# Kernel optimization log

Hardware: AMD Instinct MI355X
Metric: run time of the kernel (lower is better)

## Reference

```python
import jax, jax.numpy as jnp
import numpy as np

B, N, D = 1, 65536, 1024
H = 512
R = 16  # num_regions
C = 2   # num_classes

def _gelu(x):
    return jax.nn.gelu(x, approximate=False)  # torch nn.GELU default is exact erf

def setup_inputs() -> dict:
    key = jax.random.key(0)
    ks = jax.random.split(key, 16)
    s = 0.02
    return {
        "embeddings": jax.random.normal(ks[0], (B, N, D), dtype=jnp.float32),
        # region_encoder: Linear(D,H) + GELU (dropout=0 in eval)
        "W1": jax.random.normal(ks[1], (D, H), dtype=jnp.float32) * s,
        "b1": jnp.zeros((H,), dtype=jnp.float32),
        # region_attention: Linear(H,H//2) -> tanh -> Linear(H//2,1)
        "Wa1": jax.random.normal(ks[2], (H, H // 2), dtype=jnp.float32) * s,
        "ba1": jnp.zeros((H // 2,), dtype=jnp.float32),
        "Wa2": jax.random.normal(ks[3], (H // 2, 1), dtype=jnp.float32) * s,
        "ba2": jnp.zeros((1,), dtype=jnp.float32),
        # slide_encoder: Linear(H,H) + GELU
        "Ws": jax.random.normal(ks[4], (H, H), dtype=jnp.float32) * s,
        "bs": jnp.zeros((H,), dtype=jnp.float32),
        # slide_attention
        "Wsa1": jax.random.normal(ks[5], (H, H // 2), dtype=jnp.float32) * s,
        "bsa1": jnp.zeros((H // 2,), dtype=jnp.float32),
        "Wsa2": jax.random.normal(ks[6], (H // 2, 1), dtype=jnp.float32) * s,
        "bsa2": jnp.zeros((1,), dtype=jnp.float32),
        # classifier: Linear(H,H//2) -> GELU -> Linear(H//2,C)
        "Wc1": jax.random.normal(ks[7], (H, H // 2), dtype=jnp.float32) * s,
        "bc1": jnp.zeros((H // 2,), dtype=jnp.float32),
        "Wc2": jax.random.normal(ks[8], (H // 2, C), dtype=jnp.float32) * s,
        "bc2": jnp.zeros((C,), dtype=jnp.float32),
    }

def reference(embeddings, W1, b1, Wa1, ba1, Wa2, ba2, Ws, bs, Wsa1, bsa1, Wsa2, bsa2, Wc1, bc1, Wc2, bc2):
    b, n, d = embeddings.shape
    m = n // R  # patches per region
    # coords=None path: region_ids[i] = i % R, so region r holds indices r, r+R, ...
    # Equivalent regrouping via reshape+transpose: (B, M, R, D) -> (B, R, M, D)
    x = embeddings.reshape(b, m, R, d).transpose(0, 2, 1, 3)
    # region encoder
    region_emb = _gelu(jnp.einsum('brmd,dh->brmh', x, W1) + b1)  # (B,R,M,H)
    # region attention pooling
    scores = jnp.einsum('brmk,ko->brmo', jnp.tanh(jnp.einsum('brmh,hk->brmk', region_emb, Wa1) + ba1), Wa2) + ba2  # (B,R,M,1)
    attn = jax.nn.softmax(scores, axis=2)
    region_features = jnp.sum(region_emb * attn, axis=2)  # (B,R,H)
    # slide encoder + attention pooling over regions
    slide_emb = _gelu(jnp.einsum('brh,hg->brg', region_features, Ws) + bs)  # (B,R,H)
    sattn = jnp.einsum('brk,ko->bro', jnp.tanh(jnp.einsum('brh,hk->brk', slide_emb, Wsa1) + bsa1), Wsa2) + bsa2  # (B,R,1)
    sweights = jax.nn.softmax(sattn, axis=1)
    slide_rep = jnp.sum(slide_emb * sweights, axis=1)  # (B,H)
    # classifier
    logits = _gelu(slide_rep @ Wc1 + bc1) @ Wc2 + bc2  # (B,C)
    return logits
```

## Files before the change

kernel.cpp:

```cpp
#include <hip/hip_runtime.h>

#define NTOK 65536
#define DIN  1024
#define H    512
#define HH   256
#define NREG 16
#define MPR  4096

__device__ __forceinline__ unsigned short f2bf(float f) {
  unsigned u = __float_as_uint(f);
  u += 0x7fffu + ((u >> 16) & 1u);
  return (unsigned short)(u >> 16);
}
__device__ __forceinline__ float bf2f(unsigned short s) {
  return __uint_as_float(((unsigned)s) << 16);
}
__device__ __forceinline__ float gelu_exact(float x) {
  return 0.5f * x * (1.0f + erff(x * 0.70710678118654752440f));
}
__device__ __forceinline__ unsigned cvt_pk_bf16(float lo, float hi) {
  unsigned r;
  asm("v_cvt_pk_bf16_f32 %0, %1, %2" : "=v"(r) : "v"(lo), "v"(hi));
  return r;
}
__device__ __forceinline__ unsigned short f2bf_hw(float f) {
  unsigned r;
  asm("v_cvt_pk_bf16_f32 %0, %1, %2" : "=v"(r) : "v"(f), "v"(f));
  return (unsigned short)r;
}
__device__ __forceinline__ float fast_tanh(float x) {
  float e = __expf(2.0f * x);
  return 1.0f - 2.0f * __builtin_amdgcn_rcpf(e + 1.0f);
}

typedef __attribute__((ext_vector_type(8))) short shortx8;
typedef __attribute__((ext_vector_type(4))) float floatx4;
typedef __attribute__((ext_vector_type(4))) unsigned int uintx4;

__device__ __forceinline__ void gl_lds16(const void* g, void* l) {
  __builtin_amdgcn_global_load_lds(
      (const __attribute__((address_space(1))) void*)g,
      (__attribute__((address_space(3))) void*)l, 16, 0, 0);
}

__device__ __forceinline__ int swz8(int row, int seg) {
  return (row * 4 + (seg ^ ((row >> 1) & 3))) * 8;
}

__global__ __launch_bounds__(256) void k0_prep(const float* __restrict__ W1,
                                               const float* __restrict__ Wa1,
                                               unsigned short* __restrict__ W1t,
                                               unsigned short* __restrict__ Wa1t) {
  int idx = blockIdx.x * 256 + threadIdx.x;
  if (idx < DIN * H) {
    int n = idx >> 10, k = idx & 1023;
    W1t[idx] = f2bf(W1[k * H + n]);
  } else {
    int i2 = idx - DIN * H;
    int n = i2 >> 9, k = i2 & 511;
    Wa1t[i2] = f2bf(Wa1[k * HH + n]);
  }
}

__global__ __launch_bounds__(512) void k1_gemm1(const float* __restrict__ X,
                                                const unsigned short* __restrict__ W1t,
                                                const float* __restrict__ b1,
                                                unsigned short* __restrict__ Eb) {
  __shared__ __align__(16) short lA[128 * 32];
  __shared__ __align__(16) short lB[512 * 32];
  const int tid = threadIdx.x;
  const int rowBase = blockIdx.x * 128;
  const int lane = tid & 63;
  const int wave = tid >> 6;
  const int wr = wave >> 2, wc = wave & 3;
  const int l15 = lane & 15, quad = lane >> 4;

  floatx4 acc[4][8] = {};

  const int arow = tid >> 2, aseg = tid & 3;
  const float* aSrc = X + (size_t)(rowBase + arow) * DIN + aseg * 8;
  short* aDst = &lA[swz8(arow, aseg)];

  for (int kb = 0; kb < DIN; kb += 32) {
    __syncthreads();
#pragma unroll
    for (int s = 0; s < 4; s++) {
      int c = tid + s * 512;
      int n = c >> 2, slot = c & 3;
      int seg = slot ^ ((n >> 1) & 3);
      gl_lds16(W1t + (size_t)n * DIN + kb + seg * 8, &lB[c * 8]);
    }
    {
      const floatx4* src = (const floatx4*)(aSrc + kb);
      floatx4 f0 = src[0], f1 = src[1];
      uintx4 u;
      u[0] = cvt_pk_bf16(f0[0], f0[1]);
      u[1] = cvt_pk_bf16(f0[2], f0[3]);
      u[2] = cvt_pk_bf16(f1[0], f1[1]);
      u[3] = cvt_pk_bf16(f1[2], f1[3]);
      *(uintx4*)aDst = u;
    }
    __syncthreads();
    shortx8 aF[4], bF[8];
#pragma unroll
    for (int i = 0; i < 4; i++) {
      int r = wr * 64 + i * 16 + l15;
      aF[i] = *(const shortx8*)(&lA[swz8(r, quad)]);
    }
#pragma unroll
    for (int j = 0; j < 8; j++) {
      int r = wc * 128 + j * 16 + l15;
      bF[j] = *(const shortx8*)(&lB[swz8(r, quad)]);
    }
#pragma unroll
    for (int i = 0; i < 4; i++)
#pragma unroll
      for (int j = 0; j < 8; j++)
        acc[i][j] = __builtin_amdgcn_mfma_f32_16x16x32_bf16(aF[i], bF[j], acc[i][j], 0, 0, 0);
  }

  const int row0 = rowBase + wr * 64;
#pragma unroll
  for (int j = 0; j < 8; j++) {
    int col = wc * 128 + j * 16 + l15;
    float bias = b1[col];
#pragma unroll
    for (int i = 0; i < 4; i++) {
      int rb = row0 + i * 16 + quad * 4;
#pragma unroll
      for (int v = 0; v < 4; v++) {
        float x = acc[i][j][v] + bias;
        Eb[(size_t)(rb + v) * H + col] = f2bf_hw(gelu_exact(x));
      }
    }
  }
}

__global__ __launch_bounds__(256) void k2_gemm2(const unsigned short* __restrict__ Eb,
                                                const unsigned short* __restrict__ Wa1t,
                                                const float* __restrict__ ba1,
                                                const float* __restrict__ Wa2,
                                                float* __restrict__ scores) {
  __shared__ __align__(16) short lA[128 * 32];
  __shared__ __align__(16) short lB[128 * 32];
  const int tid = threadIdx.x;
  const int colBase = blockIdx.x * 128;
  const int rowBase = blockIdx.y * 128;
  const int lane = tid & 63;
  const int wave = tid >> 6;
  const int wr = wave >> 1, wc = wave & 1;
  const int l15 = lane & 15, quad = lane >> 4;

  floatx4 acc[4][4] = {};

  for (int kb = 0; kb < H; kb += 32) {
    __syncthreads();
#pragma unroll
    for (int s = 0; s < 2; s++) {
      int c = tid + s * 256;
      int n = c >> 2, slot = c & 3;
      int seg = slot ^ ((n >> 1) & 3);
      gl_lds16(Eb + (size_t)(rowBase + n) * H + kb + seg * 8, &lA[c * 8]);
      gl_lds16(Wa1t + (size_t)(colBase + n) * H + kb + seg * 8, &lB[c * 8]);
    }
    __syncthreads();
    shortx8 aF[4], bF[4];
#pragma unroll
    for (int i = 0; i < 4; i++) {
      int r = wr * 64 + i * 16 + l15;
      aF[i] = *(const shortx8*)(&lA[swz8(r, quad)]);
    }
#pragma unroll
    for (int j = 0; j < 4; j++) {
      int r = wc * 64 + j * 16 + l15;
      bF[j] = *(const shortx8*)(&lB[swz8(r, quad)]);
    }
#pragma unroll
    for (int i = 0; i < 4; i++)
#pragma unroll
      for (int j = 0; j < 4; j++)
        acc[i][j] = __builtin_amdgcn_mfma_f32_16x16x32_bf16(aF[i], bF[j], acc[i][j], 0, 0, 0);
  }

  float p[4][4];
#pragma unroll
  for (int i = 0; i < 4; i++)
#pragma unroll
    for (int v = 0; v < 4; v++) p[i][v] = 0.0f;
#pragma unroll
  for (int j = 0; j < 4; j++) {
    int col = colBase + wc * 64 + j * 16 + l15;
    float bias = ba1[col];
    float wa2 = Wa2[col];
#pragma unroll
    for (int i = 0; i < 4; i++)
#pragma unroll
      for (int v = 0; v < 4; v++)
        p[i][v] += fast_tanh(acc[i][j][v] + bias) * wa2;
  }
#pragma unroll
  for (int i = 0; i < 4; i++)
#pragma unroll
    for (int v = 0; v < 4; v++) {
      float t = p[i][v];
      t += __shfl_xor(t, 1, 16);
      t += __shfl_xor(t, 2, 16);
      t += __shfl_xor(t, 4, 16);
      t += __shfl_xor(t, 8, 16);
      p[i][v] = t;
    }
  if (l15 == 0) {
    int row0 = rowBase + wr * 64 + quad * 4;
#pragma unroll
    for (int i = 0; i < 4; i++)
#pragma unroll
      for (int v = 0; v < 4; v++)
        atomicAdd(&scores[row0 + i * 16 + v], p[i][v]);
  }
}

__global__ __launch_bounds__(256) void k3a_softmax(const float* __restrict__ scores,
                                                   float* __restrict__ wts) {
  const int r = blockIdx.x, tid = threadIdx.x;
  __shared__ float red[256];
  float m = -1e30f;
  for (int j = tid; j < MPR; j += 256) m = fmaxf(m, scores[r + NREG * j]);
  red[tid] = m;
  __syncthreads();
  for (int s = 128; s > 0; s >>= 1) {
    if (tid < s) red[tid] = fmaxf(red[tid], red[tid + s]);
    __syncthreads();
  }
  float mx = red[0];
  __syncthreads();
  float sum = 0.0f;
  for (int j = tid; j < MPR; j += 256) sum += expf(scores[r + NREG * j] - mx);
  red[tid] = sum;
  __syncthreads();
  for (int s = 128; s > 0; s >>= 1) {
    if (tid < s) red[tid] += red[tid + s];
    __syncthreads();
  }
  float inv = 1.0f / red[0];
  for (int j = tid; j < MPR; j += 256)
    wts[r + NREG * j] = expf(scores[r + NREG * j] - mx) * inv;
}

__global__ __launch_bounds__(256) void k3b_wsum(const unsigned short* __restrict__ Eb,
                                                const float* __restrict__ wts,
                                                float* __restrict__ rf) {
  const int r = blockIdx.y;
  const int mc = blockIdx.x;
  const int tid = threadIdx.x;
  float a0 = 0.0f, a1 = 0.0f;
  for (int j = mc * 128; j < mc * 128 + 128; j++) {
    int n = r + NREG * j;
    float w = wts[n];
    unsigned v = *(const unsigned*)(Eb + (size_t)n * H + tid * 2);
    a0 += w * bf2f((unsigned short)(v & 0xffffu));
    a1 += w * bf2f((unsigned short)(v >> 16));
  }
  atomicAdd(&rf[r * H + tid * 2], a0);
  atomicAdd(&rf[r * H + tid * 2 + 1], a1);
}

__global__ __launch_bounds__(256) void k4a_slide(const float* __restrict__ rf,
                                                 const float* __restrict__ Ws,
                                                 const float* __restrict__ bs,
                                                 float* __restrict__ se) {
  const int r = blockIdx.x, tid = threadIdx.x;
  __shared__ float lrf[H];
  lrf[tid] = rf[r * H + tid];
  lrf[tid + 256] = rf[r * H + tid + 256];
  __syncthreads();
  float a0 = 0.0f, a1 = 0.0f;
  for (int k = 0; k < H; k++) {
    float x = lrf[k];
    a0 += x * Ws[k * H + tid];
    a1 += x * Ws[k * H + tid + 256];
  }
  se[r * H + tid] = gelu_exact(a0 + bs[tid]);
  se[r * H + tid + 256] = gelu_exact(a1 + bs[tid + 256]);
}

__global__ __launch_bounds__(256) void k4b_sscore(const float* __restrict__ se,
                                                  const float* __restrict__ Wsa1,
                                                  const float* __restrict__ bsa1,
                                                  const float* __restrict__ Wsa2,
                                                  const float* __restrict__ bsa2,
                                                  float* __restrict__ ss) {
  const int r = blockIdx.x, tid = threadIdx.x;
  __shared__ float lse[H];
  __shared__ float red[256];
  lse[tid] = se[r * H + tid];
  lse[tid + 256] = se[r * H + tid + 256];
  __syncthreads();
  float a = 0.0f;
  for (int k = 0; k < H; k++) a += lse[k] * Wsa1[k * HH + tid];
  red[tid] = tanhf(a + bsa1[tid]) * Wsa2[tid];
  __syncthreads();
  for (int s = 128; s > 0; s >>= 1) {
    if (tid < s) red[tid] += red[tid + s];
    __syncthreads();
  }
  if (tid == 0) ss[r] = red[0] + bsa2[0];
}

__global__ __launch_bounds__(256) void k4c_final(const float* __restrict__ se,
                                                 const float* __restrict__ ss,
                                                 const float* __restrict__ Wc1,
                                                 const float* __restrict__ bc1,
                                                 const float* __restrict__ Wc2,
                                                 const float* __restrict__ bc2,
                                                 float* __restrict__ out) {
  const int tid = threadIdx.x;
  __shared__ float srep[H];
  __shared__ float r0[256], r1[256];
  float mx = -1e30f;
  for (int i = 0; i < NREG; i++) mx = fmaxf(mx, ss[i]);
  float wv[NREG];
  float den = 0.0f;
  for (int i = 0; i < NREG; i++) { wv[i] = expf(ss[i] - mx); den += wv[i]; }
  float inv = 1.0f / den;
  float s0 = 0.0f, s1 = 0.0f;
  for (int i = 0; i < NREG; i++) {
    float w = wv[i] * inv;
    s0 += w * se[i * H + tid];
    s1 += w * se[i * H + tid + 256];
  }
  srep[tid] = s0;
  srep[tid + 256] = s1;
  __syncthreads();
  float a = 0.0f;
  for (int k = 0; k < H; k++) a += srep[k] * Wc1[k * HH + tid];
  float g = gelu_exact(a + bc1[tid]);
  r0[tid] = g * Wc2[tid * 2];
  r1[tid] = g * Wc2[tid * 2 + 1];
  __syncthreads();
  for (int s = 128; s > 0; s >>= 1) {
    if (tid < s) { r0[tid] += r0[tid + s]; r1[tid] += r1[tid + s]; }
    __syncthreads();
  }
  if (tid == 0) {
    out[0] = r0[0] + bc2[0];
    out[1] = r1[0] + bc2[1];
  }
}

extern "C" void kernel_launch(void* const* d_in, const int* in_sizes, int n_in,
                              void* d_out, int out_size, void* d_ws, size_t ws_size,
                              hipStream_t stream) {
  const float* X    = (const float*)d_in[0];
  const float* W1   = (const float*)d_in[1];
  const float* b1   = (const float*)d_in[2];
  const float* Wa1  = (const float*)d_in[3];
  const float* ba1  = (const float*)d_in[4];
  const float* Wa2  = (const float*)d_in[5];
  const float* Ws   = (const float*)d_in[7];
  const float* bs   = (const float*)d_in[8];
  const float* Wsa1 = (const float*)d_in[9];
  const float* bsa1 = (const float*)d_in[10];
  const float* Wsa2 = (const float*)d_in[11];
  const float* bsa2 = (const float*)d_in[12];
  const float* Wc1  = (const float*)d_in[13];
  const float* bc1  = (const float*)d_in[14];
  const float* Wc2  = (const float*)d_in[15];
  const float* bc2  = (const float*)d_in[16];
  float* out = (float*)d_out;

  char* ws = (char*)d_ws;
  constexpr size_t OFF_W1T  = 0;
  constexpr size_t OFF_WA1T = OFF_W1T + (size_t)H * DIN * 2;
  constexpr size_t OFF_EB   = OFF_WA1T + (size_t)HH * H * 2;
  constexpr size_t OFF_SC   = OFF_EB + (size_t)NTOK * H * 2;
  constexpr size_t OFF_RF   = OFF_SC + (size_t)NTOK * 4;
  constexpr size_t OFF_WT   = OFF_RF + (size_t)NREG * H * 4;
  constexpr size_t OFF_SE   = OFF_WT + (size_t)NTOK * 4;
  constexpr size_t OFF_SS   = OFF_SE + (size_t)NREG * H * 4;

  unsigned short* W1t  = (unsigned short*)(ws + OFF_W1T);
  unsigned short* Wa1t = (unsigned short*)(ws + OFF_WA1T);
  unsigned short* Eb   = (unsigned short*)(ws + OFF_EB);
  float* scores = (float*)(ws + OFF_SC);
  float* rf     = (float*)(ws + OFF_RF);
  float* wts    = (float*)(ws + OFF_WT);
  float* se     = (float*)(ws + OFF_SE);
  float* ssb    = (float*)(ws + OFF_SS);

  hipMemsetAsync(scores, 0, (size_t)NTOK * 4 + (size_t)NREG * H * 4, stream);

  k0_prep<<<(DIN * H + HH * H) / 256, 256, 0, stream>>>(W1, Wa1, W1t, Wa1t);
  k1_gemm1<<<512, 512, 0, stream>>>(X, W1t, b1, Eb);
  k2_gemm2<<<dim3(2, 512), 256, 0, stream>>>(Eb, Wa1t, ba1, Wa2, scores);
  k3a_softmax<<<NREG, 256, 0, stream>>>(scores, wts);
  k3b_wsum<<<dim3(32, NREG), 256, 0, stream>>>(Eb, wts, rf);
  k4a_slide<<<NREG, 256, 0, stream>>>(rf, Ws, bs, se);
  k4b_sscore<<<NREG, 256, 0, stream>>>(se, Wsa1, bsa1, Wsa2, bsa2, ssb);
  k4c_final<<<1, 256, 0, stream>>>(se, ssb, Wc1, bc1, Wc2, bc2, out);
}
```

Before: 619.1 us.

## Double-buffer LDS in both GEMMs and compute full score rows per block

Adds ping-pong LDS buffers to the first and second GEMM so global loads for the next K-slice are issued before the MFMAs on the current one, cutting one barrier per iteration. The second GEMM now covers all 256 hidden columns per 512-thread block and reduces the partial scores in LDS, writing them directly instead of using atomicAdd. That also lets the scores memset be dropped. The cost is twice the LDS footprint, which may lower occupancy, most of all in the first GEMM.

```diff
diff --git a/kernel.cpp b/kernel.cpp
--- a/kernel.cpp
+++ b/kernel.cpp
@@ -66,8 +66,8 @@
                                                 const unsigned short* __restrict__ W1t,
                                                 const float* __restrict__ b1,
                                                 unsigned short* __restrict__ Eb) {
-  __shared__ __align__(16) short lA[128 * 32];
-  __shared__ __align__(16) short lB[512 * 32];
+  __shared__ __align__(16) short lA[2][128 * 32];
+  __shared__ __align__(16) short lB[2][512 * 32];
   const int tid = threadIdx.x;
   const int rowBase = blockIdx.x * 128;
   const int lane = tid & 63;
@@ -79,44 +79,65 @@
 
   const int arow = tid >> 2, aseg = tid & 3;
   const float* aSrc = X + (size_t)(rowBase + arow) * DIN + aseg * 8;
-  short* aDst = &lA[swz8(arow, aseg)];
-
-  for (int kb = 0; kb < DIN; kb += 32) {
-    __syncthreads();
-#pragma unroll
-    for (int s = 0; s < 4; s++) {
-      int c = tid + s * 512;
-      int n = c >> 2, slot = c & 3;
-      int seg = slot ^ ((n >> 1) & 3);
-      gl_lds16(W1t + (size_t)n * DIN + kb + seg * 8, &lB[c * 8]);
+  const int aOff = swz8(arow, aseg);
+
+#pragma unroll
+  for (int s = 0; s < 4; s++) {
+    int c = tid + s * 512;
+    int n = c >> 2;
+    int seg = (c & 3) ^ ((n >> 1) & 3);
+    gl_lds16(W1t + (size_t)n * DIN + seg * 8, &lB[0][c * 8]);
+  }
+  {
+    const floatx4* src = (const floatx4*)aSrc;
+    floatx4 f0 = src[0], f1 = src[1];
+    uintx4 u;
+    u[0] = cvt_pk_bf16(f0[0], f0[1]);
+    u[1] = cvt_pk_bf16(f0[2], f0[3]);
+    u[2] = cvt_pk_bf16(f1[0], f1[1]);
+    u[3] = cvt_pk_bf16(f1[2], f1[3]);
+    *(uintx4*)(&lA[0][aOff]) = u;
+  }
+  __syncthreads();
+
+#pragma unroll 1
+  for (int t = 0; t < 32; ++t) {
+    const int cur = t & 1, nxt = cur ^ 1;
+    floatx4 f0, f1;
+    if (t < 31) {
+      const int kb = (t + 1) * 32;
+#pragma unroll
+      for (int s = 0; s < 4; s++) {
+        int c = tid + s * 512;
+        int n = c >> 2;
+        int seg = (c & 3) ^ ((n >> 1) & 3);
+        gl_lds16(W1t + (size_t)n * DIN + kb + seg * 8, &lB[nxt][c * 8]);
+      }
+      const floatx4* src = (const floatx4*)(aSrc + kb);
+      f0 = src[0];
+      f1 = src[1];
     }
-    {
-      const floatx4* src = (const floatx4*)(aSrc + kb);
-      floatx4 f0 = src[0], f1 = src[1];
+    shortx8 aF[4], bF[8];
+#pragma unroll
+    for (int i = 0; i < 4; i++)
+      aF[i] = *(const shortx8*)(&lA[cur][swz8(wr * 64 + i * 16 + l15, quad)]);
+#pragma unroll
+    for (int j = 0; j < 8; j++)
+      bF[j] = *(const shortx8*)(&lB[cur][swz8(wc * 128 + j * 16 + l15, quad)]);
+#pragma unroll
+    for (int i = 0; i < 4; i++)
+#pragma unroll
+      for (int j = 0; j < 8; j++)
+        acc[i][j] = __builtin_amdgcn_mfma_f32_16x16x32_bf16(aF[i], bF[j], acc[i][j], 0, 0, 0);
+    if (t < 31) {
       uintx4 u;
       u[0] = cvt_pk_bf16(f0[0], f0[1]);
       u[1] = cvt_pk_bf16(f0[2], f0[3]);
       u[2] = cvt_pk_bf16(f1[0], f1[1]);
       u[3] = cvt_pk_bf16(f1[2], f1[3]);
-      *(uintx4*)aDst = u;
+      *(uintx4*)(&lA[nxt][aOff]) = u;
+      __syncthreads();
     }
-    __syncthreads();
-    shortx8 aF[4], bF[8];
-#pragma unroll
-    for (int i = 0; i < 4; i++) {
-      int r = wr * 64 + i * 16 + l15;
-      aF[i] = *(const shortx8*)(&lA[swz8(r, quad)]);
-    }
-#pragma unroll
-    for (int j = 0; j < 8; j++) {
-      int r = wc * 128 + j * 16 + l15;
-      bF[j] = *(const shortx8*)(&lB[swz8(r, quad)]);
-    }
-#pragma unroll
-    for (int i = 0; i < 4; i++)
-#pragma unroll
-      for (int j = 0; j < 8; j++)
-        acc[i][j] = __builtin_amdgcn_mfma_f32_16x16x32_bf16(aF[i], bF[j], acc[i][j], 0, 0, 0);
   }
 
   const int row0 = rowBase + wr * 64;
@@ -136,50 +157,70 @@
   }
 }
 
-__global__ __launch_bounds__(256) void k2_gemm2(const unsigned short* __restrict__ Eb,
+__global__ __launch_bounds__(512) void k2_gemm2(const unsigned short* __restrict__ Eb,
                                                 const unsigned short* __restrict__ Wa1t,
                                                 const float* __restrict__ ba1,
                                                 const float* __restrict__ Wa2,
                                                 float* __restrict__ scores) {
-  __shared__ __align__(16) short lA[128 * 32];
-  __shared__ __align__(16) short lB[128 * 32];
+  __shared__ __align__(16) short lA[2][128 * 32];
+  __shared__ __align__(16) short lB[2][256 * 32];
+  __shared__ float part[4][128];
   const int tid = threadIdx.x;
-  const int colBase = blockIdx.x * 128;
-  const int rowBase = blockIdx.y * 128;
+  const int rowBase = blockIdx.x * 128;
   const int lane = tid & 63;
   const int wave = tid >> 6;
-  const int wr = wave >> 1, wc = wave & 1;
+  const int wr = wave >> 2, wc = wave & 3;
   const int l15 = lane & 15, quad = lane >> 4;
 
   floatx4 acc[4][4] = {};
 
-  for (int kb = 0; kb < H; kb += 32) {
-    __syncthreads();
-#pragma unroll
-    for (int s = 0; s < 2; s++) {
-      int c = tid + s * 256;
-      int n = c >> 2, slot = c & 3;
-      int seg = slot ^ ((n >> 1) & 3);
-      gl_lds16(Eb + (size_t)(rowBase + n) * H + kb + seg * 8, &lA[c * 8]);
-      gl_lds16(Wa1t + (size_t)(colBase + n) * H + kb + seg * 8, &lB[c * 8]);
+  {
+    int c = tid;
+    int n = c >> 2;
+    int seg = (c & 3) ^ ((n >> 1) & 3);
+    gl_lds16(Eb + (size_t)(rowBase + n) * H + seg * 8, &lA[0][c * 8]);
+  }
+#pragma unroll
+  for (int s = 0; s < 2; s++) {
+    int c = tid + s * 512;
+    int n = c >> 2;
+    int seg = (c & 3) ^ ((n >> 1) & 3);
+    gl_lds16(Wa1t + (size_t)n * H + seg * 8, &lB[0][c * 8]);
+  }
+  __syncthreads();
+
+#pragma unroll 1
+  for (int t = 0; t < 16; ++t) {
+    const int cur = t & 1, nxt = cur ^ 1;
+    if (t < 15) {
+      const int kb = (t + 1) * 32;
+      {
+        int c = tid;
+        int n = c >> 2;
+        int seg = (c & 3) ^ ((n >> 1) & 3);
+        gl_lds16(Eb + (size_t)(rowBase + n) * H + kb + seg * 8, &lA[nxt][c * 8]);
+      }
+#pragma unroll
+      for (int s = 0; s < 2; s++) {
+        int c = tid + s * 512;
+        int n = c >> 2;
+        int seg = (c & 3) ^ ((n >> 1) & 3);
+        gl_lds16(Wa1t + (size_t)n * H + kb + seg * 8, &lB[nxt][c * 8]);
+      }
     }
-    __syncthreads();
     shortx8 aF[4], bF[4];
 #pragma unroll
-    for (int i = 0; i < 4; i++) {
-      int r = wr * 64 + i * 16 + l15;
-      aF[i] = *(const shortx8*)(&lA[swz8(r, quad)]);
-    }
-#pragma unroll
-    for (int j = 0; j < 4; j++) {
-      int r = wc * 64 + j * 16 + l15;
-      bF[j] = *(const shortx8*)(&lB[swz8(r, quad)]);
-    }
+    for (int i = 0; i < 4; i++)
+      aF[i] = *(const shortx8*)(&lA[cur][swz8(wr * 64 + i * 16 + l15, quad)]);
+#pragma unroll
+    for (int j = 0; j < 4; j++)
+      bF[j] = *(const shortx8*)(&lB[cur][swz8(wc * 64 + j * 16 + l15, quad)]);
 #pragma unroll
     for (int i = 0; i < 4; i++)
 #pragma unroll
       for (int j = 0; j < 4; j++)
         acc[i][j] = __builtin_amdgcn_mfma_f32_16x16x32_bf16(aF[i], bF[j], acc[i][j], 0, 0, 0);
+    if (t < 15) __syncthreads();
   }
 
   float p[4][4];
@@ -189,7 +230,7 @@
     for (int v = 0; v < 4; v++) p[i][v] = 0.0f;
 #pragma unroll
   for (int j = 0; j < 4; j++) {
-    int col = colBase + wc * 64 + j * 16 + l15;
+    int col = wc * 64 + j * 16 + l15;
     float bias = ba1[col];
     float wa2 = Wa2[col];
 #pragma unroll
@@ -210,13 +251,15 @@
       p[i][v] = t;
     }
   if (l15 == 0) {
-    int row0 = rowBase + wr * 64 + quad * 4;
 #pragma unroll
     for (int i = 0; i < 4; i++)
 #pragma unroll
       for (int v = 0; v < 4; v++)
-        atomicAdd(&scores[row0 + i * 16 + v], p[i][v]);
-  }
+        part[wc][wr * 64 + i * 16 + quad * 4 + v] = p[i][v];
+  }
+  __syncthreads();
+  if (tid < 128)
+    scores[rowBase + tid] = part[0][tid] + part[1][tid] + part[2][tid] + part[3][tid];
 }
 
 __global__ __launch_bounds__(256) void k3a_softmax(const float* __restrict__ scores,
@@ -387,11 +430,11 @@
   float* se     = (float*)(ws + OFF_SE);
   float* ssb    = (float*)(ws + OFF_SS);
 
-  hipMemsetAsync(scores, 0, (size_t)NTOK * 4 + (size_t)NREG * H * 4, stream);
+  hipMemsetAsync(rf, 0, (size_t)NREG * H * 4, stream);
 
   k0_prep<<<(DIN * H + HH * H) / 256, 256, 0, stream>>>(W1, Wa1, W1t, Wa1t);
   k1_gemm1<<<512, 512, 0, stream>>>(X, W1t, b1, Eb);
-  k2_gemm2<<<dim3(2, 512), 256, 0, stream>>>(Eb, Wa1t, ba1, Wa2, scores);
+  k2_gemm2<<<512, 512, 0, stream>>>(Eb, Wa1t, ba1, Wa2, scores);
   k3a_softmax<<<NREG, 256, 0, stream>>>(scores, wts);
   k3b_wsum<<<dim3(32, NREG), 256, 0, stream>>>(Eb, wts, rf);
   k4a_slide<<<NREG, 256, 0, stream>>>(rf, Ws, bs, se);
```

Measured after the change: 624.5 us. No clear change (+0.9%).
